# Kernel optimization log

Measured on AMD Instinct MI355X. Metric: run time of the kernel, lower is better.

Reference implementation:

```python
import jax, jax.numpy as jnp
import numpy as np

EPS_FEAT = 1e-4   # numerical stabilizer inside FAVOR+ features
EPS_DEN = 0.01    # denominator clamp in attention normalization


def _favorp(data, proj, is_query):
    # data: [b,h,n,d], proj: [h,j,d]
    d = data.shape[-1]
    data_normalizer = d ** (-0.25)
    ratio = proj.shape[-2] ** (-0.5)
    data_dash = jnp.einsum('bhnd,hjd->bhnj', data_normalizer * data, proj)
    diag = jnp.sum(data * data, axis=-1, keepdims=True) * (0.5 * data_normalizer * data_normalizer)
    if is_query:
        stab = jax.lax.stop_gradient(jnp.max(data_dash, axis=-1, keepdims=True))
    else:
        stab = jax.lax.stop_gradient(jnp.max(data_dash, axis=(-1, -2), keepdims=True))
    return ratio * jnp.exp(data_dash - diag - stab) + EPS_FEAT


def setup_inputs() -> dict:
    key = jax.random.key(0)
    ks = jax.random.split(key, 6)
    B, N, D, H, J = 4, 4096, 1024, 16, 64
    dh = D // H
    s = 0.02
    return {
        'query': jax.random.normal(ks[0], (B, N, D), dtype=jnp.float32),
        'Wq': jax.random.normal(ks[1], (D, D), dtype=jnp.float32) * s,
        'bq': jnp.zeros((D,), dtype=jnp.float32),
        'Wk': jax.random.normal(ks[2], (D, D), dtype=jnp.float32) * s,
        'bk': jnp.zeros((D,), dtype=jnp.float32),
        'Wv': jax.random.normal(ks[3], (D, D), dtype=jnp.float32) * s,
        'bv': jnp.zeros((D,), dtype=jnp.float32),
        'Wo': jax.random.normal(ks[4], (D, D), dtype=jnp.float32) * s,
        'bo': jnp.zeros((D,), dtype=jnp.float32),
        'proj': jax.random.normal(ks[5], (H, J, dh), dtype=jnp.float32),
    }


def reference(query, Wq, bq, Wk, bk, Wv, bv, Wo, bo, proj):
    B, N, D = query.shape
    H = proj.shape[0]
    dh = D // H

    def split_heads(x):  # [b,n,(h d)] -> [b,h,n,d]
        return x.reshape(B, N, H, dh).transpose(0, 2, 1, 3)

    q = split_heads(query @ Wq.T + bq)
    k = split_heads(query @ Wk.T + bk)
    v = split_heads(query @ Wv.T + bv)

    q_prime = _favorp(q, proj, is_query=True)   # [b,h,n,j]
    k_prime = _favorp(k, proj, is_query=False)  # [b,h,n,j]

    # Non-causal linear attention: O(n * j * d)
    kv = jnp.einsum('bhnj,bhnd->bhjd', k_prime, v)
    qkv = jnp.einsum('bhnj,bhjd->bhnd', q_prime, kv)
    normalizer = jnp.einsum('bhnj,bhj->bhn', q_prime, k_prime.sum(axis=2))
    out = qkv / jnp.clip(normalizer, EPS_DEN, None)[..., None]

    out = out.transpose(0, 2, 1, 3).reshape(B, N, D)  # [b,n,(h d)]
    return out @ Wo.T + bo
```

## Files before the change

kernel.cpp:

```cpp
#include <hip/hip_runtime.h>
#include <hip/hip_bf16.h>

using floatx4 = __attribute__((ext_vector_type(4))) float;
using bf16x8  = __attribute__((ext_vector_type(8))) __bf16;
using uintx4  = __attribute__((ext_vector_type(4))) unsigned int;

#define DEV __device__ __forceinline__

DEV unsigned short f2bf(float f){
  unsigned u = __float_as_uint(f);
  u = (u + 0x7FFFu + ((u >> 16) & 1u)) >> 16;
  return (unsigned short)u;
}
DEV float bf2f(unsigned short h){ return __uint_as_float(((unsigned)h) << 16); }

DEV void gload_lds16(const void* g, void* l){
  __builtin_amdgcn_global_load_lds((const __attribute__((address_space(1))) void*)g,
                                   (__attribute__((address_space(3))) void*)l, 16, 0, 0);
}

DEV void atomicMaxF(float* a, float v){
  if (v >= 0.f) atomicMax((int*)a, __float_as_int(v));
  else          atomicMin((unsigned int*)a, __float_as_uint(v));
}

#define SBAR do{ __builtin_amdgcn_sched_barrier(0); __builtin_amdgcn_s_barrier(); \
                 __builtin_amdgcn_sched_barrier(0); }while(0)

__global__ __launch_bounds__(256) void k_prep(
    const float* __restrict__ query, const float* __restrict__ Wq,
    const float* __restrict__ Wk, const float* __restrict__ Wv,
    const float* __restrict__ Wo, const float* __restrict__ proj,
    unsigned short* __restrict__ qbf, unsigned short* __restrict__ wqb,
    unsigned short* __restrict__ wkb, unsigned short* __restrict__ wvb,
    unsigned short* __restrict__ wob, unsigned short* __restrict__ pjb,
    float* __restrict__ esum, float* __restrict__ vsum, float* __restrict__ stab)
{
  const int bid = blockIdx.x, tid = threadIdx.x;
  const float* s; unsigned short* d; int i, stride, n4;
  if (bid < 1024){ s = query; d = qbf; i = bid*256 + tid; stride = 262144; n4 = 4194304; }
  else if (bid < 1280){
    int w = (bid - 1024) >> 6;
    s = (w==0)?Wq:(w==1)?Wk:(w==2)?Wv:Wo;
    d = (w==0)?wqb:(w==1)?wkb:(w==2)?wvb:wob;
    i = ((bid-1024)&63)*256 + tid; stride = 16384; n4 = 262144;
  } else if (bid < 1296){ s = proj; d = pjb; i = (bid-1280)*256 + tid; stride = 4096; n4 = 16384; }
  else {
    for (int k = tid; k < 4096; k += 256){ esum[k] = 0.f; vsum[k] = 0.f; }
    if (tid < 64) stab[tid] = -1e30f;
    return;
  }
  for (; i < n4; i += stride){
    float4 v = ((const float4*)s)[i];
    ushort4 o;
    o.x = f2bf(v.x); o.y = f2bf(v.y); o.z = f2bf(v.z); o.w = f2bf(v.w);
    ((ushort4*)d)[i] = o;
  }
}

template<int OUTMODE>
__global__ __launch_bounds__(512, 1) void gemm256(
    const unsigned short* __restrict__ A,
    const unsigned short* __restrict__ W,
    const float* __restrict__ bias0, const float* __restrict__ bias1,
    const float* __restrict__ bias2,
    unsigned short* __restrict__ out0, unsigned short* __restrict__ out1,
    unsigned short* __restrict__ out2,
    float* __restrict__ outf, int M, int Nout, int K)
{
  __shared__ __align__(16) char lds[131072];
  const int tid  = threadIdx.x;
  const int wid  = tid >> 6, lane = tid & 63;
  const int wr   = wid >> 2, wc = wid & 3;
  const int fr   = lane & 15, kch = lane >> 4;
  const int m0   = blockIdx.x * 256, n0 = blockIdx.y * 256;
  const int NU   = (K >> 6) * 4;
  const size_t Kb = (size_t)K * 2;

  const int ssw = (((lane & 3) ^ ((lane >> 3) & 3))) * 16;
  const char* Arow = (const char*)A + (size_t)(m0 + wid*16 + (lane >> 2))*Kb + ssw;
  const char* Brow = (const char*)W + (size_t)(n0 + wid*16 + (lane >> 2))*Kb + ssw;

  auto stage = [&](int u){
    if (u >= NU) return;
    int T = u >> 2, q = u & 3, isB = q & 1, s = q >> 1;
    char* dst = lds + (T & 1)*65536 + isB*32768 + s*16384 + wid*1024;
    const char* src = (isB ? Brow : Arow) + (size_t)T*128 + s*64;
    gload_lds16(src, dst);
    gload_lds16(src + 128*Kb, dst + 8192);
  };

  stage(0); stage(1); stage(2); stage(3);

  const int rkey = (fr >> 1) & 3;
  const int aBase = (wr*128 + fr)*64 + (kch ^ rkey)*16;
  const int bBase = 32768 + (wc*64 + fr)*64 + (kch ^ rkey)*16;
  floatx4 acc[8][4] = {};
  bf16x8 a[4], bq[4];

  const int NTt = K >> 6;
  for (int T = 0; T < NTt; ++T){
    const char* buf = lds + (T & 1)*65536;
    asm volatile("s_waitcnt vmcnt(4)" ::: "memory");
    SBAR;
    #pragma unroll
    for (int mt = 0; mt < 4; ++mt) a[mt]  = *(const bf16x8*)(buf + aBase + mt*1024);
    #pragma unroll
    for (int nt = 0; nt < 4; ++nt) bq[nt] = *(const bf16x8*)(buf + bBase + nt*1024);
    stage(T*4 + 4);
    __builtin_amdgcn_s_setprio(1);
    #pragma unroll
    for (int mt = 0; mt < 4; ++mt)
      #pragma unroll
      for (int nt = 0; nt < 4; ++nt)
        acc[mt][nt] = __builtin_amdgcn_mfma_f32_16x16x32_bf16(a[mt], bq[nt], acc[mt][nt], 0, 0, 0);
    __builtin_amdgcn_s_setprio(0);
    #pragma unroll
    for (int mt = 0; mt < 4; ++mt) a[mt] = *(const bf16x8*)(buf + aBase + (4+mt)*1024);
    stage(T*4 + 5);
    __builtin_amdgcn_s_setprio(1);
    #pragma unroll
    for (int mt = 0; mt < 4; ++mt)
      #pragma unroll
      for (int nt = 0; nt < 4; ++nt)
        acc[4+mt][nt] = __builtin_amdgcn_mfma_f32_16x16x32_bf16(a[mt], bq[nt], acc[4+mt][nt], 0, 0, 0);
    __builtin_amdgcn_s_setprio(0);
    if (T + 1 < NTt) asm volatile("s_waitcnt vmcnt(4)" ::: "memory");
    else             asm volatile("s_waitcnt vmcnt(0)" ::: "memory");
    SBAR;
    #pragma unroll
    for (int mt = 0; mt < 4; ++mt) a[mt]  = *(const bf16x8*)(buf + 16384 + aBase + mt*1024);
    #pragma unroll
    for (int nt = 0; nt < 4; ++nt) bq[nt] = *(const bf16x8*)(buf + 16384 + bBase + nt*1024);
    stage(T*4 + 6);
    __builtin_amdgcn_s_setprio(1);
    #pragma unroll
    for (int mt = 0; mt < 4; ++mt)
      #pragma unroll
      for (int nt = 0; nt < 4; ++nt)
        acc[mt][nt] = __builtin_amdgcn_mfma_f32_16x16x32_bf16(a[mt], bq[nt], acc[mt][nt], 0, 0, 0);
    __builtin_amdgcn_s_setprio(0);
    #pragma unroll
    for (int mt = 0; mt < 4; ++mt) a[mt] = *(const bf16x8*)(buf + 16384 + aBase + (4+mt)*1024);
    stage(T*4 + 7);
    __builtin_amdgcn_s_setprio(1);
    #pragma unroll
    for (int mt = 0; mt < 4; ++mt)
      #pragma unroll
      for (int nt = 0; nt < 4; ++nt)
        acc[4+mt][nt] = __builtin_amdgcn_mfma_f32_16x16x32_bf16(a[mt], bq[nt], acc[4+mt][nt], 0, 0, 0);
    __builtin_amdgcn_s_setprio(0);
  }

  SBAR;
  if (OUTMODE == 0){
    const int which = n0 >> 10;
    const float* bb = (which == 0) ? bias0 : (which == 1) ? bias1 : bias2;
    unsigned short* oo = (which == 0) ? out0 : (which == 1) ? out1 : out2;
    unsigned short* Lt = (unsigned short*)lds;
    #pragma unroll
    for (int nf = 0; nf < 4; ++nf){
      int col = wc*64 + nf*16 + fr;
      float bv = bb[(n0 + col) & 1023];
      #pragma unroll
      for (int mf = 0; mf < 8; ++mf)
        #pragma unroll
        for (int r = 0; r < 4; ++r){
          int row = wr*128 + mf*16 + kch*4 + r;
          Lt[row*256 + (col ^ (((row >> 2) & 3) << 4))] = f2bf(acc[mf][nf][r] + bv);
        }
    }
    SBAR;
    const int orow = tid >> 5, oj = tid & 31;
    #pragma unroll
    for (int p = 0; p < 16; ++p){
      int row = p*16 + orow;
      uintx4 v = *(const uintx4*)(Lt + row*256 + ((oj*8) ^ (((row >> 2) & 3) << 4)));
      *(uintx4*)(oo + (size_t)(m0 + row)*1024 + (n0 & 1023) + oj*8) = v;
    }
  } else {
    float* Lf = (float*)lds;
    #pragma unroll
    for (int p = 0; p < 2; ++p){
      if (wr == p){
        #pragma unroll
        for (int nf = 0; nf < 4; ++nf){
          int col = wc*64 + nf*16 + fr;
          float bv = bias0[n0 + col];
          #pragma unroll
          for (int mf = 0; mf < 8; ++mf)
            #pragma unroll
            for (int r = 0; r < 4; ++r){
              int row = mf*16 + kch*4 + r;
              Lf[row*256 + (col ^ (((row >> 2) & 3) << 4))] = acc[mf][nf][r] + bv;
            }
        }
      }
      SBAR;
      const int oj = tid & 63;
      #pragma unroll
      for (int pp = 0; pp < 16; ++pp){
        int row = pp*8 + wid;
        uintx4 v = *(const uintx4*)(Lf + row*256 + ((oj*4) ^ (((row >> 2) & 3) << 4)));
        *(uintx4*)(outf + (size_t)(m0 + p*128 + row)*Nout + n0 + oj*4) = v;
      }
      SBAR;
    }
  }
}

#define CS 0.35355339059327373f

__global__ __launch_bounds__(256) void k_favor_k(const unsigned short* __restrict__ Kb,
                                                 const unsigned short* __restrict__ Pb,
                                                 unsigned short* __restrict__ Ktp,
                                                 float* __restrict__ esum,
                                                 float* __restrict__ stab,
                                                 int Nn, int D, int H)
{
  __shared__ __align__(16) unsigned short Qs[128*64];
  __shared__ __align__(16) unsigned short Ps[64*64];
  __shared__ __align__(16) unsigned short T[64*136];
  __shared__ float diag_s[128];
  __shared__ float wm[4];
  const int tid = threadIdx.x, wave = tid >> 6, lane = tid & 63;
  const int bh = blockIdx.y, h = bh % H, b = bh / H;
  const int n0 = blockIdx.x * 128;
  const int fr = lane & 15, kch = lane >> 4;
  const int sr = lane >> 3, sc = (lane & 7) * 8;
  #pragma unroll
  for (int q = 0; q < 4; ++q){
    int seg = wave*4 + q;
    gload_lds16(Kb + ((size_t)b*Nn + n0 + seg*8 + sr)*D + h*64 + sc, (char*)Qs + seg*1024);
  }
  #pragma unroll
  for (int q = 0; q < 2; ++q){
    int seg = wave*2 + q;
    gload_lds16(Pb + (size_t)h*4096 + seg*512 + lane*8, (char*)Ps + seg*1024);
  }
  __syncthreads();
  {
    int row = tid >> 1, half = tid & 1;
    float s = 0.f;
    for (int i = 0; i < 32; ++i){
      int d = half*32 + ((row + i) & 31);
      float x = bf2f(Qs[row*64 + d]);
      s += x*x;
    }
    float o = __shfl_xor(s, 1);
    if (half == 0) diag_s[row] = 0.0625f * (s + o);
  }
  floatx4 acc[2][4] = {};
  #pragma unroll
  for (int ks = 0; ks < 2; ++ks){
    bf16x8 af[2], bfr[4];
    #pragma unroll
    for (int m = 0; m < 2; ++m)
      af[m] = *(const bf16x8*)((const char*)Qs + (wave*32 + m*16 + fr)*128 + ks*64 + kch*16);
    #pragma unroll
    for (int n = 0; n < 4; ++n)
      bfr[n] = *(const bf16x8*)((const char*)Ps + (n*16 + fr)*128 + ks*64 + kch*16);
    #pragma unroll
    for (int m = 0; m < 2; ++m)
      #pragma unroll
      for (int n = 0; n < 4; ++n)
        acc[m][n] = __builtin_amdgcn_mfma_f32_16x16x32_bf16(af[m], bfr[n], acc[m][n], 0, 0, 0);
  }
  __syncthreads();
  float mx = -1e30f;
  #pragma unroll
  for (int m = 0; m < 2; ++m)
  #pragma unroll
  for (int r = 0; r < 4; ++r){
    int row = wave*32 + m*16 + kch*4 + r;
    float dg = diag_s[row];
    #pragma unroll
    for (int n = 0; n < 4; ++n){
      float dd = CS * acc[m][n][r];
      mx = fmaxf(mx, dd);
      float e = 0.125f * __expf(dd - dg);
      T[(n*16 + fr)*136 + row] = f2bf(e);
    }
  }
  #pragma unroll
  for (int off = 1; off < 64; off <<= 1) mx = fmaxf(mx, __shfl_xor(mx, off));
  if (lane == 0) wm[wave] = mx;
  __syncthreads();
  if (tid == 0) atomicMaxF(&stab[bh], fmaxf(fmaxf(wm[0],wm[1]), fmaxf(wm[2],wm[3])));
  {
    int j = tid >> 2, part = tid & 3;
    float s = 0.f;
    for (int i = 0; i < 32; ++i) s += bf2f(T[j*136 + part*32 + i]);
    s += __shfl_xor(s, 1); s += __shfl_xor(s, 2);
    if (part == 0) atomicAdd(&esum[bh*64 + j], s);
  }
  for (int it = 0; it < 4; ++it){
    int sidx = it*256 + tid;
    int j = sidx >> 4, nn = (sidx & 15) * 8;
    uintx4 v = *(const uintx4*)((const char*)T + (j*136 + nn)*2);
    *(uintx4*)(Ktp + ((size_t)bh*64 + j)*Nn + n0 + nn) = v;
  }
}

__global__ __launch_bounds__(256) void k_vtrans(const unsigned short* __restrict__ Vb,
                                                unsigned short* __restrict__ Vtp,
                                                float* __restrict__ vsum,
                                                int Nn, int D, int H)
{
  __shared__ __align__(16) unsigned short T[64*136];
  const int tid = threadIdx.x;
  const int bh = blockIdx.y, h = bh % H, b = bh / H;
  const int n0 = blockIdx.x * 128;
  for (int it = 0; it < 4; ++it){
    int s8 = it*256 + tid;
    int n = s8 >> 3, d0 = (s8 & 7) * 8;
    uintx4 v = *(const uintx4*)(Vb + ((size_t)b*Nn + n0 + n)*D + h*64 + d0);
    const unsigned short* us = (const unsigned short*)&v;
    #pragma unroll
    for (int ii = 0; ii < 8; ++ii) T[(d0+ii)*136 + n] = us[ii];
  }
  __syncthreads();
  {
    int d = tid >> 2, part = tid & 3;
    float s = 0.f;
    for (int i = 0; i < 32; ++i) s += bf2f(T[d*136 + part*32 + i]);
    s += __shfl_xor(s, 1); s += __shfl_xor(s, 2);
    if (part == 0) atomicAdd(&vsum[bh*64 + d], s);
  }
  for (int it = 0; it < 4; ++it){
    int sidx = it*256 + tid;
    int d = sidx >> 4, nn = (sidx & 15) * 8;
    uintx4 v = *(const uintx4*)((const char*)T + (d*136 + nn)*2);
    *(uintx4*)(Vtp + ((size_t)bh*64 + d)*Nn + n0 + nn) = v;
  }
}

__global__ __launch_bounds__(256) void k_kv(const unsigned short* __restrict__ Ktp,
                                            const unsigned short* __restrict__ Vtp,
                                            float* __restrict__ kvp, int Nn)
{
  __shared__ __align__(16) unsigned short As[64*32];
  __shared__ __align__(16) unsigned short Bs[64*32];
  const int tid = threadIdx.x, wave = tid >> 6, lane = tid & 63;
  const int ks = blockIdx.x, bh = blockIdx.y;
  const int base = ks * 512;
  const int fr = lane & 15, kch = lane >> 4;
  const int sr = lane >> 2, sc = (lane & 3) * 8;
  floatx4 acc[4] = {};
  for (int kk = 0; kk < 512; kk += 32){
    gload_lds16(Ktp + ((size_t)bh*64 + wave*16 + sr)*Nn + base + kk + sc, (char*)As + wave*1024);
    gload_lds16(Vtp + ((size_t)bh*64 + wave*16 + sr)*Nn + base + kk + sc, (char*)Bs + wave*1024);
    __syncthreads();
    bf16x8 af = *(const bf16x8*)((const char*)As + (wave*16 + fr)*64 + kch*16);
    #pragma unroll
    for (int n = 0; n < 4; ++n){
      bf16x8 bfr = *(const bf16x8*)((const char*)Bs + (n*16 + fr)*64 + kch*16);
      acc[n] = __builtin_amdgcn_mfma_f32_16x16x32_bf16(af, bfr, acc[n], 0, 0, 0);
    }
    __syncthreads();
  }
  #pragma unroll
  for (int n = 0; n < 4; ++n)
  #pragma unroll
  for (int r = 0; r < 4; ++r){
    int j = wave*16 + kch*4 + r;
    int d = n*16 + fr;
    kvp[((size_t)(ks*64 + bh)*64 + j)*64 + d] = acc[n][r];
  }
}

__global__ __launch_bounds__(256) void k_kvred(const float* __restrict__ kvp,
                                               const float* __restrict__ stab,
                                               const float* __restrict__ esum,
                                               const float* __restrict__ vsum,
                                               unsigned short* __restrict__ Kvt,
                                               float* __restrict__ ksumf){
  const int bh = blockIdx.x, tid = threadIdx.x;
  const float s = __expf(-stab[bh]);
  for (int i = 0; i < 16; ++i){
    int idx = i*256 + tid;
    int j = idx >> 6, d = idx & 63;
    float sum = 0.f;
    #pragma unroll
    for (int ks = 0; ks < 8; ++ks) sum += kvp[((size_t)(ks*64 + bh)*64 + j)*64 + d];
    Kvt[((size_t)bh*64 + d)*64 + j] = f2bf(s*sum + 1e-4f*vsum[bh*64 + d]);
  }
  if (tid < 64) ksumf[bh*64 + tid] = s*esum[bh*64 + tid] + 0.4096f;
}

__global__ __launch_bounds__(256) void k_qattn(const unsigned short* __restrict__ Qb,
                                               const unsigned short* __restrict__ Pb,
                                               const unsigned short* __restrict__ Kvt,
                                               const float* __restrict__ ksumf,
                                               unsigned short* __restrict__ att,
                                               int Nn, int D, int H)
{
  __shared__ __align__(16) unsigned short Qs[128*64];
  __shared__ __align__(16) unsigned short Ps[64*64];
  __shared__ __align__(16) unsigned short Ks[64*64];
  __shared__ __align__(16) unsigned short Q2[128*64];
  __shared__ float ksum_s[64];
  __shared__ float diag_s[128];
  __shared__ float nrm[128];
  const int tid = threadIdx.x, wave = tid >> 6, lane = tid & 63;
  const int bh = blockIdx.y, h = bh % H, b = bh / H;
  const int n0 = blockIdx.x * 128;
  const int fr = lane & 15, kch = lane >> 4;
  const int sr = lane >> 3, sc = (lane & 7) * 8;
  #pragma unroll
  for (int q = 0; q < 4; ++q){
    int seg = wave*4 + q;
    gload_lds16(Qb + ((size_t)b*Nn + n0 + seg*8 + sr)*D + h*64 + sc, (char*)Qs + seg*1024);
  }
  #pragma unroll
  for (int q = 0; q < 2; ++q){
    int seg = wave*2 + q;
    gload_lds16(Pb + (size_t)h*4096 + seg*512 + lane*8, (char*)Ps + seg*1024);
    gload_lds16(Kvt + (size_t)bh*4096 + seg*512 + lane*8, (char*)Ks + seg*1024);
  }
  if (tid < 64) ksum_s[tid] = ksumf[bh*64 + tid];
  __syncthreads();
  {
    int row = tid >> 1, half = tid & 1;
    float s = 0.f;
    for (int i = 0; i < 32; ++i){
      int d = half*32 + ((row + i) & 31);
      float x = bf2f(Qs[row*64 + d]);
      s += x*x;
    }
    float o = __shfl_xor(s, 1);
    if (half == 0) diag_s[row] = 0.0625f * (s + o);
  }
  floatx4 acc[2][4] = {};
  #pragma unroll
  for (int ks = 0; ks < 2; ++ks){
    bf16x8 af[2], bfr[4];
    #pragma unroll
    for (int m = 0; m < 2; ++m)
      af[m] = *(const bf16x8*)((const char*)Qs + (wave*32 + m*16 + fr)*128 + ks*64 + kch*16);
    #pragma unroll
    for (int n = 0; n < 4; ++n)
      bfr[n] = *(const bf16x8*)((const char*)Ps + (n*16 + fr)*128 + ks*64 + kch*16);
    #pragma unroll
    for (int m = 0; m < 2; ++m)
      #pragma unroll
      for (int n = 0; n < 4; ++n)
        acc[m][n] = __builtin_amdgcn_mfma_f32_16x16x32_bf16(af[m], bfr[n], acc[m][n], 0, 0, 0);
  }
  __syncthreads();
  #pragma unroll
  for (int m = 0; m < 2; ++m)
  #pragma unroll
  for (int r = 0; r < 4; ++r){
    float mxv = -1e30f;
    #pragma unroll
    for (int n = 0; n < 4; ++n) mxv = fmaxf(mxv, acc[m][n][r]);
    mxv = fmaxf(mxv, __shfl_xor(mxv, 1));
    mxv = fmaxf(mxv, __shfl_xor(mxv, 2));
    mxv = fmaxf(mxv, __shfl_xor(mxv, 4));
    mxv = fmaxf(mxv, __shfl_xor(mxv, 8));
    int row = wave*32 + m*16 + kch*4 + r;
    float dg = diag_s[row];
    float stabv = CS * mxv;
    float qp[4], pr = 0.f;
    #pragma unroll
    for (int n = 0; n < 4; ++n){
      qp[n] = 0.125f * __expf(CS*acc[m][n][r] - dg - stabv) + 1e-4f;
      pr += qp[n] * ksum_s[n*16 + fr];
    }
    pr += __shfl_xor(pr, 1); pr += __shfl_xor(pr, 2);
    pr += __shfl_xor(pr, 4); pr += __shfl_xor(pr, 8);
    if (fr == 0) nrm[row] = fmaxf(pr, 0.01f);
    #pragma unroll
    for (int n = 0; n < 4; ++n){
      int j = n*16 + fr;
      int slot = (j >> 3) ^ (row & 7);
      ((unsigned short*)Q2)[row*64 + slot*8 + (j & 7)] = f2bf(qp[n]);
    }
  }
  __syncthreads();
  floatx4 acc2[2][4] = {};
  #pragma unroll
  for (int ks = 0; ks < 2; ++ks){
    bf16x8 af[2], bfr[4];
    #pragma unroll
    for (int m = 0; m < 2; ++m){
      int row = wave*32 + m*16 + fr;
      int slot = (ks*4 + kch) ^ (row & 7);
      af[m] = *(const bf16x8*)((const char*)Q2 + row*128 + slot*16);
    }
    #pragma unroll
    for (int n = 0; n < 4; ++n)
      bfr[n] = *(const bf16x8*)((const char*)Ks + (n*16 + fr)*128 + ks*64 + kch*16);
    #pragma unroll
    for (int m = 0; m < 2; ++m)
      #pragma unroll
      for (int n = 0; n < 4; ++n)
        acc2[m][n] = __builtin_amdgcn_mfma_f32_16x16x32_bf16(af[m], bfr[n], acc2[m][n], 0, 0, 0);
  }
  #pragma unroll
  for (int m = 0; m < 2; ++m)
  #pragma unroll
  for (int r = 0; r < 4; ++r){
    int row = wave*32 + m*16 + kch*4 + r;
    float inv = 1.0f / nrm[row];
    #pragma unroll
    for (int n = 0; n < 4; ++n){
      float v = acc2[m][n][r] * inv;
      att[((size_t)b*Nn + n0 + row)*D + h*64 + n*16 + fr] = f2bf(v);
    }
  }
}

extern "C" void kernel_launch(void* const* d_in, const int* in_sizes, int n_in,
                              void* d_out, int out_size, void* d_ws, size_t ws_size,
                              hipStream_t stream)
{
  (void)in_sizes; (void)n_in; (void)out_size; (void)ws_size;
  const float* query = (const float*)d_in[0];
  const float* Wq = (const float*)d_in[1];
  const float* bq = (const float*)d_in[2];
  const float* Wk = (const float*)d_in[3];
  const float* bk = (const float*)d_in[4];
  const float* Wv = (const float*)d_in[5];
  const float* bv = (const float*)d_in[6];
  const float* Wo = (const float*)d_in[7];
  const float* bo = (const float*)d_in[8];
  const float* proj = (const float*)d_in[9];

  const int B = 4, N = 4096, D = 1024, H = 16;
  const size_t NT = (size_t)B*N*D;

  char* ws = (char*)d_ws;
  unsigned short* qbf = (unsigned short*)ws;
  unsigned short* wqb = (unsigned short*)(ws + 33554432);
  unsigned short* wkb = wqb + 1048576;
  unsigned short* wvb = wkb + 1048576;
  unsigned short* wob = wvb + 1048576;
  unsigned short* pjb = wob + 1048576;
  unsigned short* qb  = pjb + 65536;
  unsigned short* kb  = qb + NT;
  unsigned short* vb  = kb + NT;
  unsigned short* ktp = vb + NT;
  float* kvp  = (float*)(ktp + NT);
  unsigned short* kvt = (unsigned short*)(kvp + 2097152);
  float* esum = (float*)(kvt + 262144);
  float* vsum = esum + 4096;
  float* ksumf = vsum + 4096;
  float* stab = ksumf + 4096;
  unsigned short* att = qbf;
  unsigned short* vtp = kb;

  k_prep<<<1297, 256, 0, stream>>>(query, Wq, Wk, Wv, Wo, proj,
                                   qbf, wqb, wkb, wvb, wob, pjb, esum, vsum, stab);

  gemm256<0><<<dim3(64, 12), 512, 0, stream>>>(qbf, wqb, bq, bk, bv,
                                               qb, kb, vb, nullptr, B*N, 3072, D);

  dim3 gf(32, 64);
  k_favor_k<<<gf, 256, 0, stream>>>(kb, pjb, ktp, esum, stab, N, D, H);
  k_vtrans <<<gf, 256, 0, stream>>>(vb, vtp, vsum, N, D, H);
  k_kv<<<dim3(8, 64), 256, 0, stream>>>(ktp, vtp, kvp, N);
  k_kvred<<<64, 256, 0, stream>>>(kvp, stab, esum, vsum, kvt, ksumf);
  k_qattn<<<gf, 256, 0, stream>>>(qb, pjb, kvt, ksumf, att, N, D, H);

  gemm256<1><<<dim3(64, 4), 512, 0, stream>>>(att, wob, bo, nullptr, nullptr,
                                              nullptr, nullptr, nullptr,
                                              (float*)d_out, B*N, 1024, D);
}
```

Measured before the change: 243.4 us.

## Fuse key feature map, V transpose and KV product into one kernel

```diff
diff --git a/kernel.cpp b/kernel.cpp
--- a/kernel.cpp
+++ b/kernel.cpp
@@ -211,75 +211,126 @@
 
 #define CS 0.35355339059327373f
 
-__global__ __launch_bounds__(256) void k_favor_k(const unsigned short* __restrict__ Kb,
-                                                 const unsigned short* __restrict__ Pb,
-                                                 unsigned short* __restrict__ Ktp,
-                                                 float* __restrict__ esum,
-                                                 float* __restrict__ stab,
-                                                 int Nn, int D, int H)
+__global__ __launch_bounds__(256) void k_fkv(const unsigned short* __restrict__ Kb,
+                                             const unsigned short* __restrict__ Vb,
+                                             const unsigned short* __restrict__ Pb,
+                                             float* __restrict__ kvp,
+                                             float* __restrict__ esum,
+                                             float* __restrict__ vsum,
+                                             float* __restrict__ stab,
+                                             int Nn, int D, int H)
 {
-  __shared__ __align__(16) unsigned short Qs[128*64];
+  __shared__ __align__(16) unsigned short Ks[128*64];
   __shared__ __align__(16) unsigned short Ps[64*64];
-  __shared__ __align__(16) unsigned short T[64*136];
+  __shared__ __align__(16) unsigned short Te[64*136];
+  __shared__ __align__(16) unsigned short Tv[64*136];
   __shared__ float diag_s[128];
   __shared__ float wm[4];
   const int tid = threadIdx.x, wave = tid >> 6, lane = tid & 63;
-  const int bh = blockIdx.y, h = bh % H, b = bh / H;
-  const int n0 = blockIdx.x * 128;
+  const int ksb = blockIdx.x, bh = blockIdx.y, h = bh % H, b = bh / H;
   const int fr = lane & 15, kch = lane >> 4;
   const int sr = lane >> 3, sc = (lane & 7) * 8;
-  #pragma unroll
-  for (int q = 0; q < 4; ++q){
-    int seg = wave*4 + q;
-    gload_lds16(Kb + ((size_t)b*Nn + n0 + seg*8 + sr)*D + h*64 + sc, (char*)Qs + seg*1024);
-  }
-  #pragma unroll
-  for (int q = 0; q < 2; ++q){
-    int seg = wave*2 + q;
-    gload_lds16(Pb + (size_t)h*4096 + seg*512 + lane*8, (char*)Ps + seg*1024);
-  }
-  __syncthreads();
+  float esum_r = 0.f, vsum_r = 0.f, mx = -1e30f;
+  floatx4 acc_kv[4] = {};
+
+  for (int c = 0; c < 4; ++c){
+    const int n0c = ksb*512 + c*128;
+    __syncthreads();
+    #pragma unroll
+    for (int q = 0; q < 4; ++q){
+      int seg = wave*4 + q;
+      gload_lds16(Kb + ((size_t)b*Nn + n0c + seg*8 + sr)*D + h*64 + sc, (char*)Ks + seg*1024);
+    }
+    if (c == 0){
+      #pragma unroll
+      for (int q = 0; q < 2; ++q){
+        int seg = wave*2 + q;
+        gload_lds16(Pb + (size_t)h*4096 + seg*512 + lane*8, (char*)Ps + seg*1024);
+      }
+    }
+    uintx4 vr[4];
+    #pragma unroll
+    for (int it = 0; it < 4; ++it){
+      int s8 = it*256 + tid, n = s8 >> 3, d0 = (s8 & 7)*8;
+      vr[it] = *(const uintx4*)(Vb + ((size_t)b*Nn + n0c + n)*D + h*64 + d0);
+    }
+    asm volatile("s_waitcnt vmcnt(0)" ::: "memory");
+    __syncthreads();
+    {
+      int row = tid >> 1, half = tid & 1;
+      float s = 0.f;
+      for (int i = 0; i < 32; ++i){
+        int d = half*32 + ((row + i) & 31);
+        float x = bf2f(Ks[row*64 + d]);
+        s += x*x;
+      }
+      float o = __shfl_xor(s, 1);
+      if (half == 0) diag_s[row] = 0.0625f * (s + o);
+    }
+    #pragma unroll
+    for (int it = 0; it < 4; ++it){
+      int s8 = it*256 + tid, n = s8 >> 3, d0 = (s8 & 7)*8;
+      const unsigned short* us = (const unsigned short*)&vr[it];
+      #pragma unroll
+      for (int ii = 0; ii < 8; ++ii) Tv[(d0+ii)*136 + n] = us[ii];
+    }
+    floatx4 acc[2][4] = {};
+    #pragma unroll
+    for (int ksl = 0; ksl < 2; ++ksl){
+      bf16x8 af[2], bfr[4];
+      #pragma unroll
+      for (int m = 0; m < 2; ++m)
+        af[m] = *(const bf16x8*)((const char*)Ks + (wave*32 + m*16 + fr)*128 + ksl*64 + kch*16);
+      #pragma unroll
+      for (int n = 0; n < 4; ++n)
+        bfr[n] = *(const bf16x8*)((const char*)Ps + (n*16 + fr)*128 + ksl*64 + kch*16);
+      #pragma unroll
+      for (int m = 0; m < 2; ++m)
+        #pragma unroll
+        for (int n = 0; n < 4; ++n)
+          acc[m][n] = __builtin_amdgcn_mfma_f32_16x16x32_bf16(af[m], bfr[n], acc[m][n], 0, 0, 0);
+    }
+    __syncthreads();
+    #pragma unroll
+    for (int m = 0; m < 2; ++m)
+    #pragma unroll
+    for (int r = 0; r < 4; ++r){
+      int row = wave*32 + m*16 + kch*4 + r;
+      float dg = diag_s[row];
+      #pragma unroll
+      for (int n = 0; n < 4; ++n){
+        float dd = CS * acc[m][n][r];
+        mx = fmaxf(mx, dd);
+        Te[(n*16 + fr)*136 + row] = f2bf(0.125f * __expf(dd - dg));
+      }
+    }
+    __syncthreads();
+    {
+      int j = tid >> 2, part = tid & 3;
+      float s = 0.f, s2 = 0.f;
+      for (int i = 0; i < 32; ++i){
+        s  += bf2f(Te[j*136 + part*32 + i]);
+        s2 += bf2f(Tv[j*136 + part*32 + i]);
+      }
+      esum_r += s; vsum_r += s2;
+    }
+    #pragma unroll
+    for (int nc = 0; nc < 4; ++nc){
+      bf16x8 af = *(const bf16x8*)((const char*)Te + (wave*16 + fr)*272 + nc*64 + kch*16);
+      #pragma unroll
+      for (int nf = 0; nf < 4; ++nf){
+        bf16x8 bfr = *(const bf16x8*)((const char*)Tv + (nf*16 + fr)*272 + nc*64 + kch*16);
+        acc_kv[nf] = __builtin_amdgcn_mfma_f32_16x16x32_bf16(af, bfr, acc_kv[nf], 0, 0, 0);
+      }
+    }
+  }
   {
-    int row = tid >> 1, half = tid & 1;
-    float s = 0.f;
-    for (int i = 0; i < 32; ++i){
-      int d = half*32 + ((row + i) & 31);
-      float x = bf2f(Qs[row*64 + d]);
-      s += x*x;
-    }
-    float o = __shfl_xor(s, 1);
-    if (half == 0) diag_s[row] = 0.0625f * (s + o);
-  }
-  floatx4 acc[2][4] = {};
-  #pragma unroll
-  for (int ks = 0; ks < 2; ++ks){
-    bf16x8 af[2], bfr[4];
-    #pragma unroll
-    for (int m = 0; m < 2; ++m)
-      af[m] = *(const bf16x8*)((const char*)Qs + (wave*32 + m*16 + fr)*128 + ks*64 + kch*16);
-    #pragma unroll
-    for (int n = 0; n < 4; ++n)
-      bfr[n] = *(const bf16x8*)((const char*)Ps + (n*16 + fr)*128 + ks*64 + kch*16);
-    #pragma unroll
-    for (int m = 0; m < 2; ++m)
-      #pragma unroll
-      for (int n = 0; n < 4; ++n)
-        acc[m][n] = __builtin_amdgcn_mfma_f32_16x16x32_bf16(af[m], bfr[n], acc[m][n], 0, 0, 0);
-  }
-  __syncthreads();
-  float mx = -1e30f;
-  #pragma unroll
-  for (int m = 0; m < 2; ++m)
-  #pragma unroll
-  for (int r = 0; r < 4; ++r){
-    int row = wave*32 + m*16 + kch*4 + r;
-    float dg = diag_s[row];
-    #pragma unroll
-    for (int n = 0; n < 4; ++n){
-      float dd = CS * acc[m][n][r];
-      mx = fmaxf(mx, dd);
-      float e = 0.125f * __expf(dd - dg);
-      T[(n*16 + fr)*136 + row] = f2bf(e);
+    int j = tid >> 2;
+    float s = esum_r + __shfl_xor(esum_r, 1); s += __shfl_xor(s, 2);
+    float s2 = vsum_r + __shfl_xor(vsum_r, 1); s2 += __shfl_xor(s2, 2);
+    if ((tid & 3) == 0){
+      atomicAdd(&esum[bh*64 + j], s);
+      atomicAdd(&vsum[bh*64 + j], s2);
     }
   }
   #pragma unroll
@@ -287,85 +338,12 @@
   if (lane == 0) wm[wave] = mx;
   __syncthreads();
   if (tid == 0) atomicMaxF(&stab[bh], fmaxf(fmaxf(wm[0],wm[1]), fmaxf(wm[2],wm[3])));
-  {
-    int j = tid >> 2, part = tid & 3;
-    float s = 0.f;
-    for (int i = 0; i < 32; ++i) s += bf2f(T[j*136 + part*32 + i]);
-    s += __shfl_xor(s, 1); s += __shfl_xor(s, 2);
-    if (part == 0) atomicAdd(&esum[bh*64 + j], s);
-  }
-  for (int it = 0; it < 4; ++it){
-    int sidx = it*256 + tid;
-    int j = sidx >> 4, nn = (sidx & 15) * 8;
-    uintx4 v = *(const uintx4*)((const char*)T + (j*136 + nn)*2);
-    *(uintx4*)(Ktp + ((size_t)bh*64 + j)*Nn + n0 + nn) = v;
-  }
-}
-
-__global__ __launch_bounds__(256) void k_vtrans(const unsigned short* __restrict__ Vb,
-                                                unsigned short* __restrict__ Vtp,
-                                                float* __restrict__ vsum,
-                                                int Nn, int D, int H)
-{
-  __shared__ __align__(16) unsigned short T[64*136];
-  const int tid = threadIdx.x;
-  const int bh = blockIdx.y, h = bh % H, b = bh / H;
-  const int n0 = blockIdx.x * 128;
-  for (int it = 0; it < 4; ++it){
-    int s8 = it*256 + tid;
-    int n = s8 >> 3, d0 = (s8 & 7) * 8;
-    uintx4 v = *(const uintx4*)(Vb + ((size_t)b*Nn + n0 + n)*D + h*64 + d0);
-    const unsigned short* us = (const unsigned short*)&v;
-    #pragma unroll
-    for (int ii = 0; ii < 8; ++ii) T[(d0+ii)*136 + n] = us[ii];
-  }
-  __syncthreads();
-  {
-    int d = tid >> 2, part = tid & 3;
-    float s = 0.f;
-    for (int i = 0; i < 32; ++i) s += bf2f(T[d*136 + part*32 + i]);
-    s += __shfl_xor(s, 1); s += __shfl_xor(s, 2);
-    if (part == 0) atomicAdd(&vsum[bh*64 + d], s);
-  }
-  for (int it = 0; it < 4; ++it){
-    int sidx = it*256 + tid;
-    int d = sidx >> 4, nn = (sidx & 15) * 8;
-    uintx4 v = *(const uintx4*)((const char*)T + (d*136 + nn)*2);
-    *(uintx4*)(Vtp + ((size_t)bh*64 + d)*Nn + n0 + nn) = v;
-  }
-}
-
-__global__ __launch_bounds__(256) void k_kv(const unsigned short* __restrict__ Ktp,
-                                            const unsigned short* __restrict__ Vtp,
-                                            float* __restrict__ kvp, int Nn)
-{
-  __shared__ __align__(16) unsigned short As[64*32];
-  __shared__ __align__(16) unsigned short Bs[64*32];
-  const int tid = threadIdx.x, wave = tid >> 6, lane = tid & 63;
-  const int ks = blockIdx.x, bh = blockIdx.y;
-  const int base = ks * 512;
-  const int fr = lane & 15, kch = lane >> 4;
-  const int sr = lane >> 2, sc = (lane & 3) * 8;
-  floatx4 acc[4] = {};
-  for (int kk = 0; kk < 512; kk += 32){
-    gload_lds16(Ktp + ((size_t)bh*64 + wave*16 + sr)*Nn + base + kk + sc, (char*)As + wave*1024);
-    gload_lds16(Vtp + ((size_t)bh*64 + wave*16 + sr)*Nn + base + kk + sc, (char*)Bs + wave*1024);
-    __syncthreads();
-    bf16x8 af = *(const bf16x8*)((const char*)As + (wave*16 + fr)*64 + kch*16);
-    #pragma unroll
-    for (int n = 0; n < 4; ++n){
-      bf16x8 bfr = *(const bf16x8*)((const char*)Bs + (n*16 + fr)*64 + kch*16);
-      acc[n] = __builtin_amdgcn_mfma_f32_16x16x32_bf16(af, bfr, acc[n], 0, 0, 0);
-    }
-    __syncthreads();
-  }
-  #pragma unroll
-  for (int n = 0; n < 4; ++n)
+  #pragma unroll
+  for (int nf = 0; nf < 4; ++nf)
   #pragma unroll
   for (int r = 0; r < 4; ++r){
-    int j = wave*16 + kch*4 + r;
-    int d = n*16 + fr;
-    kvp[((size_t)(ks*64 + bh)*64 + j)*64 + d] = acc[n][r];
+    int j = wave*16 + kch*4 + r, d = nf*16 + fr;
+    kvp[((size_t)(ksb*64 + bh)*64 + j)*64 + d] = acc_kv[nf][r];
   }
 }
 
@@ -541,15 +519,13 @@
   unsigned short* qb  = pjb + 65536;
   unsigned short* kb  = qb + NT;
   unsigned short* vb  = kb + NT;
-  unsigned short* ktp = vb + NT;
-  float* kvp  = (float*)(ktp + NT);
+  float* kvp  = (float*)(vb + NT);
   unsigned short* kvt = (unsigned short*)(kvp + 2097152);
   float* esum = (float*)(kvt + 262144);
   float* vsum = esum + 4096;
   float* ksumf = vsum + 4096;
   float* stab = ksumf + 4096;
   unsigned short* att = qbf;
-  unsigned short* vtp = kb;
 
   k_prep<<<1297, 256, 0, stream>>>(query, Wq, Wk, Wv, Wo, proj,
                                    qbf, wqb, wkb, wvb, wob, pjb, esum, vsum, stab);
@@ -557,12 +533,9 @@
   gemm256<0><<<dim3(64, 12), 512, 0, stream>>>(qbf, wqb, bq, bk, bv,
                                                qb, kb, vb, nullptr, B*N, 3072, D);
 
-  dim3 gf(32, 64);
-  k_favor_k<<<gf, 256, 0, stream>>>(kb, pjb, ktp, esum, stab, N, D, H);
-  k_vtrans <<<gf, 256, 0, stream>>>(vb, vtp, vsum, N, D, H);
-  k_kv<<<dim3(8, 64), 256, 0, stream>>>(ktp, vtp, kvp, N);
+  k_fkv<<<dim3(8, 64), 256, 0, stream>>>(kb, vb, pjb, kvp, esum, vsum, stab, N, D, H);
   k_kvred<<<64, 256, 0, stream>>>(kvp, stab, esum, vsum, kvt, ksumf);
-  k_qattn<<<gf, 256, 0, stream>>>(qb, pjb, kvt, ksumf, att, N, D, H);
+  k_qattn<<<dim3(32, 64), 256, 0, stream>>>(qb, pjb, kvt, ksumf, att, N, D, H);
 
   gemm256<1><<<dim3(64, 4), 512, 0, stream>>>(att, wob, bo, nullptr, nullptr,
                                               nullptr, nullptr, nullptr,
```

Measured after the change: 217.8 us. -10.5%, faster.
